# Kernel tuning notes

Hardware: AMD Instinct MI355X
Metric: run time of the kernel (lower is better)

## Reference

```python
import jax, jax.numpy as jnp
import numpy as np

C = 1.0          # ball curvature
EPS = 1e-5


def _expmap0(x):
    rc = jnp.sqrt(C)
    n = jnp.maximum(jnp.linalg.norm(x, axis=-1, keepdims=True), EPS)
    return jnp.tanh(rc * n) * x / (rc * n)


def _logmap0(y):
    rc = jnp.sqrt(C)
    n = jnp.maximum(jnp.linalg.norm(y, axis=-1, keepdims=True), EPS)
    t = jnp.minimum(rc * n, 1.0 - EPS)  # keep artanh finite
    return jnp.arctanh(t) * y / (rc * n)


def _poincare_fc(x, z, bias):
    # Shimizu et al. (HNN++) Poincare fully-connected layer.
    rc = jnp.sqrt(C)
    z_norm = jnp.maximum(jnp.linalg.norm(z, axis=0), EPS)   # (out,)
    z_unit = z / z_norm                                     # (in, out)
    drcr = 2.0 * rc * bias                                  # (out,)
    rcx = rc * x                                            # (B, in)
    cx2 = jnp.minimum(jnp.sum(rcx * rcx, axis=-1, keepdims=True), 1.0 - EPS)  # (B,1)
    # unidirectional Poincare MLR per output unit
    num = (2.0 * (rcx @ z_unit)) * jnp.cosh(drcr) - (1.0 + cx2) * jnp.sinh(drcr)
    mlr = (2.0 * z_norm / rc) * jnp.arcsinh(num / (1.0 - cx2))  # (B, out)
    # lift back to the ball
    y = jnp.sinh(rc * mlr) / rc
    return y / (1.0 + jnp.sqrt(1.0 + C * jnp.sum(y * y, axis=-1, keepdims=True)))


def setup_inputs() -> dict:
    key = jax.random.key(0)
    k1, k2, k3 = jax.random.split(key, 3)
    B, DIN, DOUT = 8192, 4096, 4096
    x = jax.random.normal(k1, (B, DIN), dtype=jnp.float32) * 0.02  # small tangent vectors
    z = jax.random.normal(k2, (DIN, DOUT), dtype=jnp.float32) * (2.0 * DIN * DOUT) ** (-0.5)
    bias = jax.random.normal(k3, (DOUT,), dtype=jnp.float32) * 0.01
    return {"x": x, "z": z, "bias": bias}


def reference(x, z, bias):
    h = _expmap0(x)                 # tangent -> ball
    y = _poincare_fc(h, z, bias)    # Mobius/Poincare linear
    return _logmap0(y)              # ball -> tangent
```

## Files before the change

kernel.cpp:

```cpp
#include <hip/hip_runtime.h>
#include <hip/hip_bf16.h>
#include <math.h>

#define EPSF 1e-5f
#define LOG2E 1.4426950408889634f
#define LN2 0.6931471805599453f

typedef __attribute__((ext_vector_type(4))) float f32x4;
typedef __attribute__((ext_vector_type(8))) short s16x8;

__device__ __forceinline__ float hw_exp2(float x) { return __builtin_amdgcn_exp2f(x); }
__device__ __forceinline__ float hw_log2(float x) { return __builtin_amdgcn_logf(x); }
__device__ __forceinline__ float fast_rcp(float x) { return __builtin_amdgcn_rcpf(x); }

__device__ __forceinline__ float block_reduce_sum_256(float s) {
  #pragma unroll
  for (int o = 32; o > 0; o >>= 1) s += __shfl_xor(s, o, 64);
  __shared__ float red[4];
  int lane = threadIdx.x & 63, wid = threadIdx.x >> 6;
  if (lane == 0) red[wid] = s;
  __syncthreads();
  return red[0] + red[1] + red[2] + red[3];
}

__device__ __forceinline__ unsigned short f2bu(float f) {
  __hip_bfloat16 b = __float2bfloat16(f);
  return __builtin_bit_cast(unsigned short, b);
}

__global__ void k_expmap(const float* __restrict__ x, __hip_bfloat16* __restrict__ h,
                         float* __restrict__ cx2, float* __restrict__ invomc, int K) {
  int row = blockIdx.x, t = threadIdx.x;
  const float4* xr = (const float4*)(x + (size_t)row * K);
  float4 v[4];
  float s = 0.f;
  #pragma unroll
  for (int i = 0; i < 4; ++i) {
    v[i] = xr[t + (i << 8)];
    s += v[i].x * v[i].x + v[i].y * v[i].y + v[i].z * v[i].z + v[i].w * v[i].w;
  }
  float nsq = block_reduce_sum_256(s);
  float n = fmaxf(sqrtf(nsq), EPSF);
  float e2 = hw_exp2(2.f * LOG2E * n);
  float th = 1.f - 2.f * fast_rcp(e2 + 1.f);
  float sc = th * fast_rcp(n);
  float hn2 = sc * sc * nsq;
  float c2 = fminf(hn2, 1.f - EPSF);
  if (t == 0) { cx2[row] = c2; invomc[row] = 1.f / (1.f - c2); }
  ushort4* hr = (ushort4*)(h + (size_t)row * K);
  #pragma unroll
  for (int i = 0; i < 4; ++i) {
    ushort4 o;
    o.x = f2bu(sc * v[i].x); o.y = f2bu(sc * v[i].y);
    o.z = f2bu(sc * v[i].z); o.w = f2bu(sc * v[i].w);
    hr[t + (i << 8)] = o;
  }
}

__global__ void k_colsq(const float* __restrict__ z, float* __restrict__ part,
                        int K, int N, int rows_per_chunk) {
  int c4 = blockIdx.x * 256 + threadIdx.x;
  int r0 = blockIdx.y * rows_per_chunk;
  const float4* z4 = (const float4*)z;
  int n4 = N >> 2;
  float4 a = {0.f, 0.f, 0.f, 0.f};
  for (int r = r0; r < r0 + rows_per_chunk; ++r) {
    float4 v = z4[(size_t)r * n4 + c4];
    a.x += v.x * v.x; a.y += v.y * v.y; a.z += v.z * v.z; a.w += v.w * v.w;
  }
  ((float4*)part)[(size_t)blockIdx.y * n4 + c4] = a;
}

__global__ void k_colfin(const float* __restrict__ part, const float* __restrict__ bias,
                         float* __restrict__ zn2, float* __restrict__ invzn,
                         float* __restrict__ ch, float* __restrict__ sh,
                         int N, int nchunk) {
  int c = blockIdx.x * 256 + threadIdx.x;
  float s = 0.f;
  for (int i = 0; i < nchunk; ++i) s += part[(size_t)i * N + c];
  float zn = fmaxf(sqrtf(s), EPSF);
  zn2[c] = 2.f * zn;
  invzn[c] = 1.f / zn;
  float d = 2.f * bias[c];
  float ep = hw_exp2(LOG2E * d);
  float em = fast_rcp(ep);
  ch[c] = 0.5f * (ep + em);
  sh[c] = 0.5f * (ep - em);
}

__global__ void k_zunitT(const float* __restrict__ z, const float* __restrict__ invzn,
                         __hip_bfloat16* __restrict__ zt, int K, int N) {
  __shared__ float tile[32][33];
  int tx = threadIdx.x, ty = threadIdx.y;
  int c0 = blockIdx.x * 32, r0 = blockIdx.y * 32;
  float inv = invzn[c0 + tx];
  #pragma unroll
  for (int i = 0; i < 4; ++i)
    tile[ty + i * 8][tx] = z[(size_t)(r0 + ty + i * 8) * N + c0 + tx] * inv;
  __syncthreads();
  #pragma unroll
  for (int i = 0; i < 4; ++i)
    zt[(size_t)(c0 + ty + i * 8) * K + r0 + tx] = __float2bfloat16(tile[tx][ty + i * 8]);
}

template<int MQ, int NQ>
__device__ __forceinline__ void mm_phase(f32x4 (&acc)[8][4], const s16x8 (&av)[4][2],
                                         const s16x8 (&bv)[4][2]) {
  #pragma unroll
  for (int i = 0; i < 4; ++i) {
    #pragma unroll
    for (int jn = 0; jn < 2; ++jn) {
      acc[MQ * 4 + i][NQ * 2 + jn] = __builtin_amdgcn_mfma_f32_16x16x32_bf16(
          bv[NQ * 2 + jn][0], av[i][0], acc[MQ * 4 + i][NQ * 2 + jn], 0, 0, 0);
      acc[MQ * 4 + i][NQ * 2 + jn] = __builtin_amdgcn_mfma_f32_16x16x32_bf16(
          bv[NQ * 2 + jn][1], av[i][1], acc[MQ * 4 + i][NQ * 2 + jn], 0, 0, 0);
    }
  }
}

__device__ __forceinline__ const char* RFL64(const char* p) {
  unsigned long long b = (unsigned long long)p;
  unsigned int lo = __builtin_amdgcn_readfirstlane((unsigned int)b);
  unsigned int hi = __builtin_amdgcn_readfirstlane((unsigned int)(b >> 32));
  return (const char*)(((unsigned long long)hi << 32) | lo);
}

__global__ __launch_bounds__(512, 1) void k_gemm_dot(
    const __hip_bfloat16* __restrict__ A,
    const __hip_bfloat16* __restrict__ Bt,
    float* __restrict__ dot, int M, int N, int K) {
  __shared__ __align__(16) char smem[131072];
  const int K2 = K * 2;
  int tid = threadIdx.x, lane = tid & 63, wid = tid >> 6;
  int wm = wid >> 2, wn = wid & 3;

  int bid = blockIdx.x;
  int cpx = gridDim.x >> 3;
  int swz = (bid & 7) * cpx + (bid >> 3);
  int nbx = N >> 8;
  int bx = swz % nbx, by = swz / nbx;
  int bm0 = by * 256, bn0 = bx * 256;

  int rr = (tid >> 2) & 15;
  int cbyte = ((tid & 3) * 16) ^ ((rr & 8) << 2);
  int kb = ((tid >> 6) & 1) * 64 + cbyte;
  int r0 = ((tid >> 7) << 4) + rr;
  unsigned int off0 = (unsigned int)(r0 * K2 + kb);
  unsigned int off1 = off0 + (unsigned int)(64 * K2);
  int ldsW = wid * 1024;

  const char* aPan0 = (const char*)A + (size_t)bm0 * K2;
  const char* aPan1 = aPan0 + (size_t)128 * K2;
  const char* bPan0 = (const char*)Bt + (size_t)bn0 * K2;
  const char* bPan1 = bPan0 + (size_t)128 * K2;

  auto STAGE = [&](const char* base, int ldsBase) {
    __builtin_amdgcn_global_load_lds(
        (const __attribute__((address_space(1))) unsigned int*)(base + off0),
        (__attribute__((address_space(3))) unsigned int*)(smem + ldsBase + ldsW), 16, 0, 0);
    __builtin_amdgcn_global_load_lds(
        (const __attribute__((address_space(1))) unsigned int*)(base + off1),
        (__attribute__((address_space(3))) unsigned int*)(smem + ldsBase + ldsW + 8192), 16, 0, 0);
  };

  int labase = (lane & 15) * 64 + (((lane >> 4) * 16) ^ ((lane & 8) << 2));
  const char* pA0 = smem + wm * 16384 + labase;
  const char* pA1 = pA0 + 65536;
  const char* pB0 = smem + 32768 + (wn >> 1) * 16384 + (wn & 1) * 8192 + labase;
  const char* pB1 = pB0 + 65536;

  s16x8 av0[4][2], av1[4][2], bv[4][2];
  f32x4 acc[8][4] = {};

#define RDA0(D) do { const char* p_ = ((D) ? pA1 : pA0); \
    _Pragma("unroll") for (int i_ = 0; i_ < 4; ++i_) { \
      av0[i_][0] = *(const s16x8*)(p_ + i_ * 2048); \
      av0[i_][1] = *(const s16x8*)(p_ + i_ * 2048 + 1024); } } while (0)
#define RDA1(D) do { const char* p_ = ((D) ? pA1 : pA0); \
    _Pragma("unroll") for (int i_ = 0; i_ < 4; ++i_) { \
      av1[i_][0] = *(const s16x8*)(p_ + 8192 + i_ * 2048); \
      av1[i_][1] = *(const s16x8*)(p_ + 8192 + i_ * 2048 + 1024); } } while (0)
#define RDB01(D) do { const char* p_ = ((D) ? pB1 : pB0); \
    _Pragma("unroll") for (int f_ = 0; f_ < 2; ++f_) { \
      bv[f_][0] = *(const s16x8*)(p_ + f_ * 2048); \
      bv[f_][1] = *(const s16x8*)(p_ + f_ * 2048 + 1024); } } while (0)
#define RDB23(D) do { const char* p_ = ((D) ? pB1 : pB0); \
    _Pragma("unroll") for (int f_ = 2; f_ < 4; ++f_) { \
      bv[f_][0] = *(const s16x8*)(p_ + f_ * 2048); \
      bv[f_][1] = *(const s16x8*)(p_ + f_ * 2048 + 1024); } } while (0)

  int NT = K >> 6;

  {
    const char* a0 = RFL64(aPan0); const char* a1 = RFL64(aPan1);
    const char* b0 = RFL64(bPan0); const char* b1 = RFL64(bPan1);
    STAGE(b0, 32768); STAGE(b1, 49152); STAGE(a0, 0); STAGE(a1, 16384);
  }
  if (NT > 1) {
    const char* a0 = RFL64(aPan0 + 128); const char* a1 = RFL64(aPan1 + 128);
    const char* b0 = RFL64(bPan0 + 128); const char* b1 = RFL64(bPan1 + 128);
    STAGE(b0, 65536 + 32768); STAGE(b1, 65536 + 49152);
    STAGE(a0, 65536); STAGE(a1, 65536 + 16384);
    asm volatile("s_waitcnt vmcnt(8)");
  } else {
    asm volatile("s_waitcnt vmcnt(0)");
  }
  __builtin_amdgcn_s_barrier();

#define KTILE(D, KT) do { \
    bool pf_ = ((KT) + 2 < NT); \
    int kOff2_ = ((KT) + 2) << 7; \
    const char* aB0_ = RFL64(aPan0 + kOff2_); \
    const char* aB1_ = RFL64(aPan1 + kOff2_); \
    const char* bB0_ = RFL64(bPan0 + kOff2_); \
    const char* bB1_ = RFL64(bPan1 + kOff2_); \
     \
    RDA0(D); RDB01(D); \
    asm volatile("s_waitcnt lgkmcnt(0)"); \
    __builtin_amdgcn_s_setprio(1); mm_phase<0, 0>(acc, av0, bv); __builtin_amdgcn_s_setprio(0); \
    __builtin_amdgcn_s_barrier(); \
     \
    RDA1(D); RDB23(D); \
    asm volatile("s_waitcnt lgkmcnt(0)"); \
    __builtin_amdgcn_s_setprio(1); mm_phase<0, 1>(acc, av0, bv); __builtin_amdgcn_s_setprio(0); \
    __builtin_amdgcn_s_barrier(); \
     \
    __builtin_amdgcn_s_setprio(1); mm_phase<1, 0>(acc, av1, bv); __builtin_amdgcn_s_setprio(0); \
    __builtin_amdgcn_s_barrier(); \
     \
    if (pf_) { STAGE(bB0_, (D) * 65536 + 32768); STAGE(bB1_, (D) * 65536 + 49152); \
               STAGE(aB0_, (D) * 65536); STAGE(aB1_, (D) * 65536 + 16384); } \
    __builtin_amdgcn_s_setprio(1); mm_phase<1, 1>(acc, av1, bv); __builtin_amdgcn_s_setprio(0); \
    if (pf_) { asm volatile("s_waitcnt vmcnt(8)"); } \
    else     { asm volatile("s_waitcnt vmcnt(0)"); } \
    __builtin_amdgcn_s_barrier(); \
  } while (0)

  for (int kt = 0; kt < NT; kt += 2) {
    KTILE(0, kt);
    KTILE(1, kt + 1);
  }
#undef KTILE
#undef RDA0
#undef RDA1
#undef RDB01
#undef RDB23

  int ml = lane & 15, ng = lane >> 4;
  #pragma unroll
  for (int fm = 0; fm < 8; ++fm) {
    int row = bm0 + wm * 128 + fm * 16 + ml;
    size_t rowo = (size_t)row * N + bn0 + wn * 64 + ng * 4;
    #pragma unroll
    for (int fn = 0; fn < 4; ++fn) {
      *(f32x4*)(dot + rowo + fn * 16) = acc[fm][fn];
    }
  }
}

__global__ void k_mlr_final(float* __restrict__ io, const float* __restrict__ cx2,
                            const float* __restrict__ invomc, const float* __restrict__ zn2,
                            const float* __restrict__ chb, const float* __restrict__ shb,
                            int N) {
  int row = blockIdx.x, t = threadIdx.x;
  float4* ior = (float4*)(io + (size_t)row * N);
  const float4* ch4 = (const float4*)chb;
  const float4* sh4 = (const float4*)shb;
  const float4* z24 = (const float4*)zn2;
  float c2 = cx2[row], inv = invomc[row];
  float opc = 1.f + c2;
  float y[4][4];
  float s = 0.f;
  #pragma unroll
  for (int i = 0; i < 4; ++i) {
    int idx = t + (i << 8);
    float4 d = ior[idx], ch = ch4[idx], sh = sh4[idx], z2 = z24[idx];
    float dq[4] = {d.x, d.y, d.z, d.w};
    float chq[4] = {ch.x, ch.y, ch.z, ch.w};
    float shq[4] = {sh.x, sh.y, sh.z, sh.w};
    float zq[4] = {z2.x, z2.y, z2.z, z2.w};
    #pragma unroll
    for (int q = 0; q < 4; ++q) {
      float u = (2.f * dq[q] * chq[q] - opc * shq[q]) * inv;
      float w = u + sqrtf(fmaf(u, u, 1.f));
      float p = hw_log2(w);
      float tq = zq[q] * p;
      float ep = hw_exp2(tq);
      float em = hw_exp2(-tq);
      float yy = 0.5f * (ep - em);
      y[i][q] = yy;
      s += yy * yy;
    }
  }
  float ny2 = block_reduce_sum_256(s);
  float ny = sqrtf(ny2);
  float sfac = fast_rcp(1.f + sqrtf(1.f + ny2));
  float w = sfac * ny;
  float nw = fmaxf(w, EPSF);
  float tt = fminf(nw, 1.f - EPSF);
  float la = 0.5f * LN2 * hw_log2((1.f + tt) * fast_rcp(1.f - tt));
  float coef = la * sfac * fast_rcp(nw);
  #pragma unroll
  for (int i = 0; i < 4; ++i) {
    int idx = t + (i << 8);
    float4 o;
    o.x = coef * y[i][0]; o.y = coef * y[i][1];
    o.z = coef * y[i][2]; o.w = coef * y[i][3];
    ior[idx] = o;
  }
}

extern "C" void kernel_launch(void* const* d_in, const int* in_sizes, int n_in,
                              void* d_out, int out_size, void* d_ws, size_t ws_size,
                              hipStream_t stream) {
  const float* x    = (const float*)d_in[0];
  const float* z    = (const float*)d_in[1];
  const float* bias = (const float*)d_in[2];
  float* out = (float*)d_out;

  int N = in_sizes[2];
  int K = in_sizes[1] / N;
  int M = in_sizes[0] / K;

  char* ws = (char*)d_ws;
  size_t o = 0;
  __hip_bfloat16* h  = (__hip_bfloat16*)(ws + o); o += (size_t)M * K * 2;
  __hip_bfloat16* zt = (__hip_bfloat16*)(ws + o); o += (size_t)N * K * 2;
  float* cx2    = (float*)(ws + o); o += (size_t)M * 4;
  float* invomc = (float*)(ws + o); o += (size_t)M * 4;
  float* part   = (float*)(ws + o); o += (size_t)32 * N * 4;
  float* zn2    = (float*)(ws + o); o += (size_t)N * 4;
  float* invzn  = (float*)(ws + o); o += (size_t)N * 4;
  float* chb    = (float*)(ws + o); o += (size_t)N * 4;
  float* shb    = (float*)(ws + o); o += (size_t)N * 4;

  const int NCH = 32;
  k_expmap<<<M, 256, 0, stream>>>(x, h, cx2, invomc, K);
  k_colsq<<<dim3(N / 1024, NCH), 256, 0, stream>>>(z, part, K, N, K / NCH);
  k_colfin<<<N / 256, 256, 0, stream>>>(part, bias, zn2, invzn, chb, shb, N, NCH);
  k_zunitT<<<dim3(N / 32, K / 32), dim3(32, 8), 0, stream>>>(z, invzn, zt, K, N);
  int grid = (M / 256) * (N / 256);
  k_gemm_dot<<<grid, 512, 0, stream>>>(h, zt, out, M, N, K);
  k_mlr_final<<<M, 256, 0, stream>>>(out, cx2, invomc, zn2, chb, shb, N);
}
```

Before: 422.8 us.

## Restructure GEMM k-loop into two-phase schedule with register double-buffered fragments

Replaces the four-phase-per-k-tile MFMA schedule, which had four barriers, with two phases and one barrier per tile. The A fragment for the next tile is read into a second register buffer while the second half of the MFMAs runs, and a partial lgkmcnt wait lets the first MFMAs start before all LDS reads return. The change also raises launch_bounds min-blocks to 2. This cuts barrier stalls and overlaps LDS reads with matrix math, at the cost of more registers and a full vmcnt(0) wait each tile, which removes some of the earlier global-load overlap. With 128 KB of shared memory per block, the occupancy hint may only add register pressure.

```diff
diff --git a/kernel.cpp b/kernel.cpp
--- a/kernel.cpp
+++ b/kernel.cpp
@@ -103,21 +103,6 @@
     zt[(size_t)(c0 + ty + i * 8) * K + r0 + tx] = __float2bfloat16(tile[tx][ty + i * 8]);
 }
 
-template<int MQ, int NQ>
-__device__ __forceinline__ void mm_phase(f32x4 (&acc)[8][4], const s16x8 (&av)[4][2],
-                                         const s16x8 (&bv)[4][2]) {
-  #pragma unroll
-  for (int i = 0; i < 4; ++i) {
-    #pragma unroll
-    for (int jn = 0; jn < 2; ++jn) {
-      acc[MQ * 4 + i][NQ * 2 + jn] = __builtin_amdgcn_mfma_f32_16x16x32_bf16(
-          bv[NQ * 2 + jn][0], av[i][0], acc[MQ * 4 + i][NQ * 2 + jn], 0, 0, 0);
-      acc[MQ * 4 + i][NQ * 2 + jn] = __builtin_amdgcn_mfma_f32_16x16x32_bf16(
-          bv[NQ * 2 + jn][1], av[i][1], acc[MQ * 4 + i][NQ * 2 + jn], 0, 0, 0);
-    }
-  }
-}
-
 __device__ __forceinline__ const char* RFL64(const char* p) {
   unsigned long long b = (unsigned long long)p;
   unsigned int lo = __builtin_amdgcn_readfirstlane((unsigned int)b);
@@ -125,7 +110,7 @@
   return (const char*)(((unsigned long long)hi << 32) | lo);
 }
 
-__global__ __launch_bounds__(512, 1) void k_gemm_dot(
+__global__ __launch_bounds__(512, 2) void k_gemm_dot(
     const __hip_bfloat16* __restrict__ A,
     const __hip_bfloat16* __restrict__ Bt,
     float* __restrict__ dot, int M, int N, int K) {
@@ -169,25 +154,35 @@
   const char* pB0 = smem + 32768 + (wn >> 1) * 16384 + (wn & 1) * 8192 + labase;
   const char* pB1 = pB0 + 65536;
 
-  s16x8 av0[4][2], av1[4][2], bv[4][2];
+  s16x8 a0f[2][4][2], a1f[2][4][2], bvf[2][4][2];
   f32x4 acc[8][4] = {};
 
-#define RDA0(D) do { const char* p_ = ((D) ? pA1 : pA0); \
+#define RD_A0(D) do { const char* p_ = ((D) ? pA1 : pA0); \
     _Pragma("unroll") for (int i_ = 0; i_ < 4; ++i_) { \
-      av0[i_][0] = *(const s16x8*)(p_ + i_ * 2048); \
-      av0[i_][1] = *(const s16x8*)(p_ + i_ * 2048 + 1024); } } while (0)
-#define RDA1(D) do { const char* p_ = ((D) ? pA1 : pA0); \
+      a0f[D][i_][0] = *(const s16x8*)(p_ + i_ * 2048); \
+      a0f[D][i_][1] = *(const s16x8*)(p_ + i_ * 2048 + 1024); } } while (0)
+#define RD_A1(D) do { const char* p_ = ((D) ? pA1 : pA0); \
     _Pragma("unroll") for (int i_ = 0; i_ < 4; ++i_) { \
-      av1[i_][0] = *(const s16x8*)(p_ + 8192 + i_ * 2048); \
-      av1[i_][1] = *(const s16x8*)(p_ + 8192 + i_ * 2048 + 1024); } } while (0)
-#define RDB01(D) do { const char* p_ = ((D) ? pB1 : pB0); \
-    _Pragma("unroll") for (int f_ = 0; f_ < 2; ++f_) { \
-      bv[f_][0] = *(const s16x8*)(p_ + f_ * 2048); \
-      bv[f_][1] = *(const s16x8*)(p_ + f_ * 2048 + 1024); } } while (0)
-#define RDB23(D) do { const char* p_ = ((D) ? pB1 : pB0); \
-    _Pragma("unroll") for (int f_ = 2; f_ < 4; ++f_) { \
-      bv[f_][0] = *(const s16x8*)(p_ + f_ * 2048); \
-      bv[f_][1] = *(const s16x8*)(p_ + f_ * 2048 + 1024); } } while (0)
+      a1f[D][i_][0] = *(const s16x8*)(p_ + 8192 + i_ * 2048); \
+      a1f[D][i_][1] = *(const s16x8*)(p_ + 8192 + i_ * 2048 + 1024); } } while (0)
+#define RD_B(D) do { const char* p_ = ((D) ? pB1 : pB0); \
+    _Pragma("unroll") for (int f_ = 0; f_ < 4; ++f_) { \
+      bvf[D][f_][0] = *(const s16x8*)(p_ + f_ * 2048); \
+      bvf[D][f_][1] = *(const s16x8*)(p_ + f_ * 2048 + 1024); } } while (0)
+#define MM_A(D) do { \
+    _Pragma("unroll") for (int i_ = 0; i_ < 4; ++i_) \
+      _Pragma("unroll") for (int f_ = 0; f_ < 4; ++f_) { \
+        acc[i_][f_] = __builtin_amdgcn_mfma_f32_16x16x32_bf16( \
+            bvf[D][f_][0], a0f[D][i_][0], acc[i_][f_], 0, 0, 0); \
+        acc[i_][f_] = __builtin_amdgcn_mfma_f32_16x16x32_bf16( \
+            bvf[D][f_][1], a0f[D][i_][1], acc[i_][f_], 0, 0, 0); } } while (0)
+#define MM_B(D) do { \
+    _Pragma("unroll") for (int i_ = 0; i_ < 4; ++i_) \
+      _Pragma("unroll") for (int f_ = 0; f_ < 4; ++f_) { \
+        acc[4 + i_][f_] = __builtin_amdgcn_mfma_f32_16x16x32_bf16( \
+            bvf[D][f_][0], a1f[D][i_][0], acc[4 + i_][f_], 0, 0, 0); \
+        acc[4 + i_][f_] = __builtin_amdgcn_mfma_f32_16x16x32_bf16( \
+            bvf[D][f_][1], a1f[D][i_][1], acc[4 + i_][f_], 0, 0, 0); } } while (0)
 
   int NT = K >> 6;
 
@@ -206,34 +201,28 @@
     asm volatile("s_waitcnt vmcnt(0)");
   }
   __builtin_amdgcn_s_barrier();
+  RD_A0(0);
 
 #define KTILE(D, KT) do { \
-    bool pf_ = ((KT) + 2 < NT); \
+    bool st_ = ((KT) + 2 < NT); \
+    bool nx_ = ((KT) + 1 < NT); \
     int kOff2_ = ((KT) + 2) << 7; \
     const char* aB0_ = RFL64(aPan0 + kOff2_); \
     const char* aB1_ = RFL64(aPan1 + kOff2_); \
     const char* bB0_ = RFL64(bPan0 + kOff2_); \
     const char* bB1_ = RFL64(bPan1 + kOff2_); \
      \
-    RDA0(D); RDB01(D); \
+    RD_B(D); RD_A1(D); \
+    asm volatile("s_waitcnt lgkmcnt(8)"); \
+    __builtin_amdgcn_s_setprio(1); MM_A(D); __builtin_amdgcn_s_setprio(0); \
     asm volatile("s_waitcnt lgkmcnt(0)"); \
-    __builtin_amdgcn_s_setprio(1); mm_phase<0, 0>(acc, av0, bv); __builtin_amdgcn_s_setprio(0); \
+    asm volatile("s_waitcnt vmcnt(0)"); \
     __builtin_amdgcn_s_barrier(); \
      \
-    RDA1(D); RDB23(D); \
-    asm volatile("s_waitcnt lgkmcnt(0)"); \
-    __builtin_amdgcn_s_setprio(1); mm_phase<0, 1>(acc, av0, bv); __builtin_amdgcn_s_setprio(0); \
-    __builtin_amdgcn_s_barrier(); \
-     \
-    __builtin_amdgcn_s_setprio(1); mm_phase<1, 0>(acc, av1, bv); __builtin_amdgcn_s_setprio(0); \
-    __builtin_amdgcn_s_barrier(); \
-     \
-    if (pf_) { STAGE(bB0_, (D) * 65536 + 32768); STAGE(bB1_, (D) * 65536 + 49152); \
+    if (st_) { STAGE(bB0_, (D) * 65536 + 32768); STAGE(bB1_, (D) * 65536 + 49152); \
                STAGE(aB0_, (D) * 65536); STAGE(aB1_, (D) * 65536 + 16384); } \
-    __builtin_amdgcn_s_setprio(1); mm_phase<1, 1>(acc, av1, bv); __builtin_amdgcn_s_setprio(0); \
-    if (pf_) { asm volatile("s_waitcnt vmcnt(8)"); } \
-    else     { asm volatile("s_waitcnt vmcnt(0)"); } \
-    __builtin_amdgcn_s_barrier(); \
+    if (nx_) { RD_A0((D) ^ 1); } \
+    __builtin_amdgcn_s_setprio(1); MM_B(D); __builtin_amdgcn_s_setprio(0); \
   } while (0)
 
   for (int kt = 0; kt < NT; kt += 2) {
@@ -241,10 +230,11 @@
     KTILE(1, kt + 1);
   }
 #undef KTILE
-#undef RDA0
-#undef RDA1
-#undef RDB01
-#undef RDB23
+#undef RD_A0
+#undef RD_A1
+#undef RD_B
+#undef MM_A
+#undef MM_B
 
   int ml = lane & 15, ng = lane >> 4;
   #pragma unroll
```

Measured after the change: 608.0 us. 43.8% more time.

## Fuse MLR elementwise into GEMM epilogue and store bf16 intermediate

Applied to the files above, without the earlier changes.

The GEMM epilogue now applies the per-element MLR transform (arcsinh, sinh) and writes y as bf16 to workspace instead of writing fp32 dot products. A new final kernel reads the bf16 y, reduces the row norm and applies the logmap scale. This removes an fp32 read of the full output in the final pass and shrinks intermediate traffic. It rounds y to bf16, which changes precision, and it depends on the workspace being large enough; otherwise it falls back to the old path.

```diff
diff --git a/kernel.cpp b/kernel.cpp
--- a/kernel.cpp
+++ b/kernel.cpp
@@ -103,21 +103,6 @@
     zt[(size_t)(c0 + ty + i * 8) * K + r0 + tx] = __float2bfloat16(tile[tx][ty + i * 8]);
 }
 
-template<int MQ, int NQ>
-__device__ __forceinline__ void mm_phase(f32x4 (&acc)[8][4], const s16x8 (&av)[4][2],
-                                         const s16x8 (&bv)[4][2]) {
-  #pragma unroll
-  for (int i = 0; i < 4; ++i) {
-    #pragma unroll
-    for (int jn = 0; jn < 2; ++jn) {
-      acc[MQ * 4 + i][NQ * 2 + jn] = __builtin_amdgcn_mfma_f32_16x16x32_bf16(
-          bv[NQ * 2 + jn][0], av[i][0], acc[MQ * 4 + i][NQ * 2 + jn], 0, 0, 0);
-      acc[MQ * 4 + i][NQ * 2 + jn] = __builtin_amdgcn_mfma_f32_16x16x32_bf16(
-          bv[NQ * 2 + jn][1], av[i][1], acc[MQ * 4 + i][NQ * 2 + jn], 0, 0, 0);
-    }
-  }
-}
-
 __device__ __forceinline__ const char* RFL64(const char* p) {
   unsigned long long b = (unsigned long long)p;
   unsigned int lo = __builtin_amdgcn_readfirstlane((unsigned int)b);
@@ -125,10 +110,16 @@
   return (const char*)(((unsigned long long)hi << 32) | lo);
 }
 
+template<int FUSE>
 __global__ __launch_bounds__(512, 1) void k_gemm_dot(
     const __hip_bfloat16* __restrict__ A,
     const __hip_bfloat16* __restrict__ Bt,
-    float* __restrict__ dot, int M, int N, int K) {
+    float* __restrict__ dotf,
+    unsigned short* __restrict__ ybf,
+    const float* __restrict__ cx2, const float* __restrict__ invomc,
+    const float* __restrict__ zn2b, const float* __restrict__ chb,
+    const float* __restrict__ shb,
+    int M, int N, int K) {
   __shared__ __align__(16) char smem[131072];
   const int K2 = K * 2;
   int tid = threadIdx.x, lane = tid & 63, wid = tid >> 6;
@@ -188,6 +179,14 @@
     _Pragma("unroll") for (int f_ = 2; f_ < 4; ++f_) { \
       bv[f_][0] = *(const s16x8*)(p_ + f_ * 2048); \
       bv[f_][1] = *(const s16x8*)(p_ + f_ * 2048 + 1024); } } while (0)
+#define MMQ(AV, NQ) do { \
+    _Pragma("unroll") for (int i_ = 0; i_ < 4; ++i_) \
+      _Pragma("unroll") for (int jn_ = 0; jn_ < 2; ++jn_) { \
+        int fr_ = (AV) * 4 + i_, fc_ = (NQ) * 2 + jn_; \
+        acc[fr_][fc_] = __builtin_amdgcn_mfma_f32_16x16x32_bf16( \
+            bv[fc_][0], ((AV) ? av1 : av0)[i_][0], acc[fr_][fc_], 0, 0, 0); \
+        acc[fr_][fc_] = __builtin_amdgcn_mfma_f32_16x16x32_bf16( \
+            bv[fc_][1], ((AV) ? av1 : av0)[i_][1], acc[fr_][fc_], 0, 0, 0); } } while (0)
 
   int NT = K >> 6;
 
@@ -217,20 +216,20 @@
      \
     RDA0(D); RDB01(D); \
     asm volatile("s_waitcnt lgkmcnt(0)"); \
-    __builtin_amdgcn_s_setprio(1); mm_phase<0, 0>(acc, av0, bv); __builtin_amdgcn_s_setprio(0); \
+    __builtin_amdgcn_s_setprio(1); MMQ(0, 0); __builtin_amdgcn_s_setprio(0); \
     __builtin_amdgcn_s_barrier(); \
      \
     RDA1(D); RDB23(D); \
     asm volatile("s_waitcnt lgkmcnt(0)"); \
-    __builtin_amdgcn_s_setprio(1); mm_phase<0, 1>(acc, av0, bv); __builtin_amdgcn_s_setprio(0); \
+    __builtin_amdgcn_s_setprio(1); MMQ(0, 1); __builtin_amdgcn_s_setprio(0); \
     __builtin_amdgcn_s_barrier(); \
      \
-    __builtin_amdgcn_s_setprio(1); mm_phase<1, 0>(acc, av1, bv); __builtin_amdgcn_s_setprio(0); \
+    __builtin_amdgcn_s_setprio(1); MMQ(1, 0); __builtin_amdgcn_s_setprio(0); \
     __builtin_amdgcn_s_barrier(); \
      \
     if (pf_) { STAGE(bB0_, (D) * 65536 + 32768); STAGE(bB1_, (D) * 65536 + 49152); \
                STAGE(aB0_, (D) * 65536); STAGE(aB1_, (D) * 65536 + 16384); } \
-    __builtin_amdgcn_s_setprio(1); mm_phase<1, 1>(acc, av1, bv); __builtin_amdgcn_s_setprio(0); \
+    __builtin_amdgcn_s_setprio(1); MMQ(1, 1); __builtin_amdgcn_s_setprio(0); \
     if (pf_) { asm volatile("s_waitcnt vmcnt(8)"); } \
     else     { asm volatile("s_waitcnt vmcnt(0)"); } \
     __builtin_amdgcn_s_barrier(); \
@@ -245,15 +244,47 @@
 #undef RDA1
 #undef RDB01
 #undef RDB23
+#undef MMQ
 
   int ml = lane & 15, ng = lane >> 4;
-  #pragma unroll
-  for (int fm = 0; fm < 8; ++fm) {
-    int row = bm0 + wm * 128 + fm * 16 + ml;
-    size_t rowo = (size_t)row * N + bn0 + wn * 64 + ng * 4;
+  int cbase = bn0 + wn * 64 + ng * 4;
+  if constexpr (FUSE == 0) {
+    #pragma unroll
+    for (int fm = 0; fm < 8; ++fm) {
+      int row = bm0 + wm * 128 + fm * 16 + ml;
+      size_t rowo = (size_t)row * N + cbase;
+      #pragma unroll
+      for (int fn = 0; fn < 4; ++fn) {
+        *(f32x4*)(dotf + rowo + fn * 16) = acc[fm][fn];
+      }
+    }
+  } else {
+    f32x4 chv[4], shv[4], znv[4];
     #pragma unroll
     for (int fn = 0; fn < 4; ++fn) {
-      *(f32x4*)(dot + rowo + fn * 16) = acc[fm][fn];
+      chv[fn] = *(const f32x4*)(chb + cbase + fn * 16);
+      shv[fn] = *(const f32x4*)(shb + cbase + fn * 16);
+      znv[fn] = *(const f32x4*)(zn2b + cbase + fn * 16);
+    }
+    #pragma unroll
+    for (int fm = 0; fm < 8; ++fm) {
+      int row = bm0 + wm * 128 + fm * 16 + ml;
+      float c2 = cx2[row], inv = invomc[row];
+      float opc = 1.f + c2;
+      size_t rowo = (size_t)row * N + cbase;
+      #pragma unroll
+      for (int fn = 0; fn < 4; ++fn) {
+        ushort4 pk;
+        #pragma unroll
+        for (int j = 0; j < 4; ++j) {
+          float u = (2.f * acc[fm][fn][j] * chv[fn][j] - opc * shv[fn][j]) * inv;
+          float wv = u + sqrtf(fmaf(u, u, 1.f));
+          float tq = znv[fn][j] * hw_log2(wv);
+          float yy = 0.5f * (hw_exp2(tq) - hw_exp2(-tq));
+          ((unsigned short*)&pk)[j] = f2bu(yy);
+        }
+        *(ushort4*)(ybf + rowo + fn * 16) = pk;
+      }
     }
   }
 }
@@ -283,11 +314,8 @@
     for (int q = 0; q < 4; ++q) {
       float u = (2.f * dq[q] * chq[q] - opc * shq[q]) * inv;
       float w = u + sqrtf(fmaf(u, u, 1.f));
-      float p = hw_log2(w);
-      float tq = zq[q] * p;
-      float ep = hw_exp2(tq);
-      float em = hw_exp2(-tq);
-      float yy = 0.5f * (ep - em);
+      float tq = zq[q] * hw_log2(w);
+      float yy = 0.5f * (hw_exp2(tq) - hw_exp2(-tq));
       y[i][q] = yy;
       s += yy * yy;
     }
@@ -307,6 +335,44 @@
     o.x = coef * y[i][0]; o.y = coef * y[i][1];
     o.z = coef * y[i][2]; o.w = coef * y[i][3];
     ior[idx] = o;
+  }
+}
+
+__global__ void k_final(const unsigned short* __restrict__ y, float* __restrict__ out,
+                        int N) {
+  int row = blockIdx.x, t = threadIdx.x;
+  const s16x8* yr = (const s16x8*)(y + (size_t)row * N);
+  float yv[16];
+  float s = 0.f;
+  #pragma unroll
+  for (int i = 0; i < 2; ++i) {
+    s16x8 v = yr[t + (i << 8)];
+    #pragma unroll
+    for (int j = 0; j < 8; ++j) {
+      unsigned int b = ((unsigned int)(unsigned short)v[j]) << 16;
+      float f = __builtin_bit_cast(float, b);
+      yv[i * 8 + j] = f;
+      s += f * f;
+    }
+  }
+  float ny2 = block_reduce_sum_256(s);
+  float ny = sqrtf(ny2);
+  float sfac = fast_rcp(1.f + sqrtf(1.f + ny2));
+  float w = sfac * ny;
+  float nw = fmaxf(w, EPSF);
+  float tt = fminf(nw, 1.f - EPSF);
+  float la = 0.5f * LN2 * hw_log2((1.f + tt) * fast_rcp(1.f - tt));
+  float coef = la * sfac * fast_rcp(nw);
+  #pragma unroll
+  for (int i = 0; i < 2; ++i) {
+    size_t base = (size_t)row * N + ((size_t)t + (i << 8)) * 8;
+    float4 o0, o1;
+    o0.x = coef * yv[i * 8 + 0]; o0.y = coef * yv[i * 8 + 1];
+    o0.z = coef * yv[i * 8 + 2]; o0.w = coef * yv[i * 8 + 3];
+    o1.x = coef * yv[i * 8 + 4]; o1.y = coef * yv[i * 8 + 5];
+    o1.z = coef * yv[i * 8 + 6]; o1.w = coef * yv[i * 8 + 7];
+    *(float4*)(out + base) = o0;
+    *(float4*)(out + base + 4) = o1;
   }
 }
 
@@ -333,6 +399,9 @@
   float* invzn  = (float*)(ws + o); o += (size_t)N * 4;
   float* chb    = (float*)(ws + o); o += (size_t)N * 4;
   float* shb    = (float*)(ws + o); o += (size_t)N * 4;
+  size_t yBytes = (size_t)M * N * 2;
+  bool fuse = (ws_size >= o + yBytes);
+  unsigned short* ybf = (unsigned short*)(ws + o);
 
   const int NCH = 32;
   k_expmap<<<M, 256, 0, stream>>>(x, h, cx2, invomc, K);
@@ -340,6 +409,13 @@
   k_colfin<<<N / 256, 256, 0, stream>>>(part, bias, zn2, invzn, chb, shb, N, NCH);
   k_zunitT<<<dim3(N / 32, K / 32), dim3(32, 8), 0, stream>>>(z, invzn, zt, K, N);
   int grid = (M / 256) * (N / 256);
-  k_gemm_dot<<<grid, 512, 0, stream>>>(h, zt, out, M, N, K);
-  k_mlr_final<<<M, 256, 0, stream>>>(out, cx2, invomc, zn2, chb, shb, N);
-}
+  if (fuse) {
+    k_gemm_dot<1><<<grid, 512, 0, stream>>>(h, zt, out, ybf, cx2, invomc, zn2, chb, shb,
+                                            M, N, K);
+    k_final<<<M, 256, 0, stream>>>(ybf, out, N);
+  } else {
+    k_gemm_dot<0><<<grid, 512, 0, stream>>>(h, zt, out, ybf, cx2, invomc, zn2, chb, shb,
+                                            M, N, K);
+    k_mlr_final<<<M, 256, 0, stream>>>(out, cx2, invomc, zn2, chb, shb, N);
+  }
+}
```

Result: no change. 422.3 us (-0.1%).
